# Performance work log

Measured on AMD Instinct MI355X. Metric: run time of the kernel, lower is better.

## Reference

```python
import jax, jax.numpy as jnp
import numpy as np

PATCH_SIZE = 3
CHANNELS = 1
SIGMA_RAW = 0.5
SIGMA_EFF = SIGMA_RAW * PATCH_SIZE ** 2  # sigma * patch_size**2 as in __init__


def setup_inputs() -> dict:
    key = jax.random.key(0)
    kx, ky = jax.random.split(key)
    N, C, H, W = 64, CHANNELS, 64, 64
    x = jax.random.normal(kx, (N, C, H, W), dtype=jnp.float32)
    y = jax.random.normal(ky, (N, C, H, W), dtype=jnp.float32)
    return {"x": x, "y": y}


def _pairwise_patch_distance(A, B):
    # A: (N_A, C, H, W), B: (N_B, C, H, W)
    N_A, C, H, W = A.shape
    N_B = B.shape[0]
    # broadcast pairwise squared pixel diffs: (N_A, N_B, C, H, W)
    pixel_diff = (A[:, None] - B[None]) ** 2
    kern = jnp.ones((1, C, PATCH_SIZE, PATCH_SIZE), dtype=A.dtype)  # OIHW
    d = jax.lax.conv_general_dilated(
        pixel_diff.reshape(N_A * N_B, C, H, W), kern,
        window_strides=(1, 1), padding='VALID',
        dimension_numbers=('NCHW', 'OIHW', 'NCHW'))
    H_new, W_new = d.shape[-2], d.shape[-1]
    return d.reshape(N_A, N_B, H_new, W_new)


def _gaussian_kernel(D):
    return jnp.exp(-D / (2.0 * SIGMA_EFF ** 2))


def _off_mean(K):
    # K: (N, N, h, w); mean over all off-diagonal (i != j) entries
    N, _, h, w = K.shape
    mask = ~jnp.eye(N, dtype=bool)
    total = jnp.sum(jnp.where(mask[:, :, None, None], K, jnp.zeros((), K.dtype)))
    count = (N * (N - 1)) * h * w
    return total / count


def reference(x, y):
    K_xx = _gaussian_kernel(_pairwise_patch_distance(x, x))
    K_xy = _gaussian_kernel(_pairwise_patch_distance(x, y))
    K_yy = _gaussian_kernel(_pairwise_patch_distance(y, y))
    return _off_mean(K_xx) - 2.0 * jnp.mean(K_xy) + _off_mean(K_yy)
```

## Files before the change

### kernel.cpp

```cpp
#include <hip/hip_runtime.h>
#include <hip/hip_fp16.h>


typedef __attribute__((ext_vector_type(4))) _Float16 half4v;
typedef __attribute__((ext_vector_type(4))) float f32x4;

#define NPOS 3844
#define WSTR 26
#define RSTR 20
#define NBLK 992

#define W_OFF (1.0 / (64.0 * 63.0 * 62.0 * 62.0))
#define W_ALL (1.0 / (64.0 * 64.0 * 62.0 * 62.0))

#if __has_builtin(__builtin_amdgcn_exp2f)
#define EXP2F(v) __builtin_amdgcn_exp2f(v)
#else
#define EXP2F(v) __expf((v) * 0.69314718055994530942f)
#endif

template<int CTRL>
__device__ __forceinline__ float dpp0_f(float v) {
    int r = __builtin_amdgcn_update_dpp(0, __float_as_int(v), CTRL, 0xf, 0xf, true);
    return __int_as_float(r);
}
template<int CTRL, int RM>
__device__ __forceinline__ float dppm_f(float v) {
    int r = __builtin_amdgcn_update_dpp(0, __float_as_int(v), CTRL, RM, 0xf, true);
    return __int_as_float(r);
}
__device__ __forceinline__ float wave_reduce_f(float v) {
    v += dpp0_f<0x111>(v);
    v += dpp0_f<0x112>(v);
    v += dpp0_f<0x114>(v);
    v += dpp0_f<0x118>(v);
    v += dppm_f<0x142, 0xa>(v);
    v += dppm_f<0x143, 0xc>(v);
    return v;
}
__device__ __forceinline__ unsigned short f16bits(float f) {
    __half h = __float2half(f);
    return *reinterpret_cast<unsigned short*>(&h);
}
__device__ __forceinline__ float f16tof(unsigned short u) {
    __half h = *reinterpret_cast<__half*>(&u);
    return __half2float(h);
}

__global__ __launch_bounds__(256, 4) void mmd_fused_kernel(
    const float* __restrict__ x, const float* __restrict__ y,
    float* __restrict__ part)
{
    const int t = threadIdx.x, wid = t >> 6, lane = t & 63;
    const int p  = blockIdx.x >> 4;
    const int qg = blockIdx.x & 15;
    const int q  = qg * 4 + wid;

    __shared__ unsigned short win[128 * WSTR];
    __shared__ unsigned short rec[4 * 128 * RSTR];
    __shared__ float pren[4 * 128];
    __shared__ float wred[3][4];

    const float NS   = -1.0f / (40.5f * 0.69314718055994530942f);
    const float M2NS = -2.0f * NS;

    {
        const int cg1 = (qg < 15) ? qg + 1 : 15;
        #pragma unroll
        for (int k = 0; k < 3; ++k) {
            int it = t + k * 256;
            int n = it / 6, rem = it % 6;
            int u = rem >> 1, cg = rem & 1;
            const float* img = (n < 64) ? (x + n * 4096) : (y + (n - 64) * 4096);
            float4 v = *reinterpret_cast<const float4*>(
                img + (p + u) * 64 + ((cg ? cg1 : qg) << 2));
            unsigned int d0 = f16bits(v.x) | ((unsigned)f16bits(v.y) << 16);
            unsigned int d1 = f16bits(v.z) | ((unsigned)f16bits(v.w) << 16);
            unsigned int* w32 = reinterpret_cast<unsigned int*>(
                &win[n * WSTR + u * 8 + cg * 4]);
            w32[0] = d0; w32[1] = d1;
        }
    }
    __syncthreads();

    #pragma unroll
    for (int k = 0; k < 2; ++k) {
        int rid = t + k * 256;
        int ql = rid >> 7, n = rid & 127;
        const unsigned short* wp = &win[n * WSTR + ql];
        unsigned short b[9];
        #pragma unroll
        for (int u = 0; u < 3; ++u) {
            b[u * 3 + 0] = wp[u * 8 + 0];
            b[u * 3 + 1] = wp[u * 8 + 1];
            b[u * 3 + 2] = wp[u * 8 + 2];
        }
        float pre = 0.f;
        #pragma unroll
        for (int e = 0; e < 9; ++e) {
            float fv = f16tof(b[e]);
            pre = fmaf(fv, fv, pre);
        }
        unsigned short* dp = &rec[(size_t)rid * RSTR];
        uint2 s0, s1, s2, s3;
        s0.x = b[0] | ((unsigned)b[1] << 16);
        s0.y = b[2] | ((unsigned)b[3] << 16);
        s1.x = b[4] | ((unsigned)b[5] << 16);
        s1.y = b[6] | ((unsigned)b[7] << 16);
        s2.x = (unsigned)b[8]; s2.y = 0u;
        s3.x = 0u;             s3.y = 0u;
        *reinterpret_cast<uint2*>(dp)      = s0;
        *reinterpret_cast<uint2*>(dp + 4)  = s1;
        *reinterpret_cast<uint2*>(dp + 8)  = s2;
        *reinterpret_cast<uint2*>(dp + 12) = s3;
        pren[rid] = pre * NS;
    }
    __syncthreads();

    const int r = lane & 15, kg = lane >> 4;
    half4v frag[8];
    #pragma unroll
    for (int g = 0; g < 8; ++g)
        frag[g] = *reinterpret_cast<const half4v*>(
            &rec[(size_t)(wid * 128 + g * 16 + r) * RSTR + kg * 4]);

    float pa[8][4], pb[8];
    #pragma unroll
    for (int g = 0; g < 8; ++g) {
        const float* pp = &pren[wid * 128 + g * 16 + kg * 4];
        pa[g][0] = pp[0]; pa[g][1] = pp[1]; pa[g][2] = pp[2]; pa[g][3] = pp[3];
        pb[g] = pren[wid * 128 + g * 16 + r];
    }

    const f32x4 zf = {0.f, 0.f, 0.f, 0.f};
    float ad0 = 0.f, ad1 = 0.f, as0 = 0.f, as1 = 0.f, ac0 = 0.f, ac1 = 0.f;

    #pragma unroll
    for (int g = 0; g < 8; ++g) {
        f32x4 c4 = __builtin_amdgcn_mfma_f32_16x16x16f16(frag[g], frag[g], zf, 0, 0, 0);
        float e = 0.f;
        #pragma unroll
        for (int m = 0; m < 4; ++m)
            e += EXP2F(fmaf(c4[m], M2NS, pa[g][m] + pb[g]));
        if (g & 1) ad1 += e; else ad0 += e;
    }

    #pragma unroll
    for (int ti = 1; ti < 8; ++ti)
        #pragma unroll
        for (int tj = 0; tj < ti; ++tj) {
            f32x4 c4 = __builtin_amdgcn_mfma_f32_16x16x16f16(frag[ti], frag[tj], zf, 0, 0, 0);
            float e = 0.f;
            #pragma unroll
            for (int m = 0; m < 4; ++m)
                e += EXP2F(fmaf(c4[m], M2NS, pa[ti][m] + pb[tj]));
            if (ti >= 4 && tj < 4) { if (tj & 1) ac1 += e; else ac0 += e; }
            else                   { if (tj & 1) as1 += e; else as0 += e; }
        }

    float acc_diag  = wave_reduce_f(ad0 + ad1);
    float acc_same  = wave_reduce_f(as0 + as1);
    float acc_cross = wave_reduce_f(ac0 + ac1);
    if (lane == 63) {
        const bool valid = (q < 62);
        wred[0][wid] = valid ? acc_diag  : 0.f;
        wred[1][wid] = valid ? acc_same  : 0.f;
        wred[2][wid] = valid ? acc_cross : 0.f;
    }
    __syncthreads();
    if (t == 0) {
        double sd = (double)((wred[0][0] + wred[0][1]) + (wred[0][2] + wred[0][3]));
        double ss = (double)((wred[1][0] + wred[1][1]) + (wred[1][2] + wred[1][3]));
        double sc = (double)((wred[2][0] + wred[2][1]) + (wred[2][2] + wred[2][3]));
        part[blockIdx.x] = (float)((sd + 2.0 * ss) * W_OFF - 2.0 * sc * W_ALL);
    }
}

__global__ __launch_bounds__(1024) void mmd_final_kernel(
    const float* __restrict__ part, float* __restrict__ out)
{
    const int t = threadIdx.x;
    double v = (t < NBLK) ? (double)part[t] : 0.0;
    #pragma unroll
    for (int off = 32; off > 0; off >>= 1)
        v += __shfl_xor(v, off);
    __shared__ double w[16];
    const int lane = t & 63, wd = t >> 6;
    if (lane == 0) w[wd] = v;
    __syncthreads();
    if (t == 0) {
        double S = 0.0;
        #pragma unroll
        for (int k = 0; k < 16; ++k) S += w[k];
        out[0] = (float)(S - 128.0 * (double)NPOS * W_OFF);
    }
}

extern "C" void kernel_launch(void* const* d_in, const int* in_sizes, int n_in,
                              void* d_out, int out_size, void* d_ws, size_t ws_size,
                              hipStream_t stream) {
    const float* x = (const float*)d_in[0];
    const float* y = (const float*)d_in[1];
    float* out  = (float*)d_out;
    float* part = (float*)d_ws;

    mmd_fused_kernel<<<NBLK, 256, 0, stream>>>(x, y, part);
    mmd_final_kernel<<<1, 1024, 0, stream>>>(part, out);
}
```

Measured before the change: 16.35 us.

## Split each column's triangular MFMA tile work across two waves per block

Doubles the block to 512 threads so two waves share each column position q. Each wave takes a balanced half of the lower-triangular 8x8 tile pairs (rows 0,1,6,7 vs 2,3,4,5, 18 tiles each). The load and record-build stages are redistributed over the larger block, and the final reduction sums eight wave partials instead of four. The aim is more parallel MFMA/exp work and shorter per-wave critical paths. The cost is more waves per block, duplicated fragment loads, and possible register and occupancy pressure at launch bounds (512,8).

```diff
diff --git a/kernel.cpp b/kernel.cpp
--- a/kernel.cpp
+++ b/kernel.cpp
@@ -47,19 +47,39 @@
     return __half2float(h);
 }
 
-__global__ __launch_bounds__(256, 4) void mmd_fused_kernel(
+template<int TI>
+__device__ __forceinline__ void do_ti(const half4v* frag, const float pa[8][4],
+                                      const float* pb, float M2NS,
+                                      float& ad, float& as, float& ac) {
+    const f32x4 zf = {0.f, 0.f, 0.f, 0.f};
+    #pragma unroll
+    for (int tj = 0; tj <= TI; ++tj) {
+        f32x4 c4 = __builtin_amdgcn_mfma_f32_16x16x16f16(frag[TI], frag[tj], zf, 0, 0, 0);
+        float e = 0.f;
+        #pragma unroll
+        for (int m = 0; m < 4; ++m)
+            e += EXP2F(fmaf(c4[m], M2NS, pa[TI][m] + pb[tj]));
+        if (tj == TI)                 ad += e;
+        else if (TI >= 4 && tj < 4)   ac += e;
+        else                          as += e;
+    }
+}
+
+__global__ __launch_bounds__(512, 8) void mmd_fused_kernel(
     const float* __restrict__ x, const float* __restrict__ y,
     float* __restrict__ part)
 {
     const int t = threadIdx.x, wid = t >> 6, lane = t & 63;
     const int p  = blockIdx.x >> 4;
     const int qg = blockIdx.x & 15;
-    const int q  = qg * 4 + wid;
+    const int pq = wid >> 1;
+    const int ws = wid & 1;
+    const int q  = qg * 4 + pq;
 
     __shared__ unsigned short win[128 * WSTR];
     __shared__ unsigned short rec[4 * 128 * RSTR];
     __shared__ float pren[4 * 128];
-    __shared__ float wred[3][4];
+    __shared__ float wred[3][8];
 
     const float NS   = -1.0f / (40.5f * 0.69314718055994530942f);
     const float M2NS = -2.0f * NS;
@@ -67,25 +87,26 @@
     {
         const int cg1 = (qg < 15) ? qg + 1 : 15;
         #pragma unroll
-        for (int k = 0; k < 3; ++k) {
-            int it = t + k * 256;
-            int n = it / 6, rem = it % 6;
-            int u = rem >> 1, cg = rem & 1;
-            const float* img = (n < 64) ? (x + n * 4096) : (y + (n - 64) * 4096);
-            float4 v = *reinterpret_cast<const float4*>(
-                img + (p + u) * 64 + ((cg ? cg1 : qg) << 2));
-            unsigned int d0 = f16bits(v.x) | ((unsigned)f16bits(v.y) << 16);
-            unsigned int d1 = f16bits(v.z) | ((unsigned)f16bits(v.w) << 16);
-            unsigned int* w32 = reinterpret_cast<unsigned int*>(
-                &win[n * WSTR + u * 8 + cg * 4]);
-            w32[0] = d0; w32[1] = d1;
-        }
-    }
-    __syncthreads();
-
-    #pragma unroll
-    for (int k = 0; k < 2; ++k) {
-        int rid = t + k * 256;
+        for (int k = 0; k < 2; ++k) {
+            int it = t + k * 512;
+            if (it < 768) {
+                int n = it / 6, rem = it % 6;
+                int u = rem >> 1, cg = rem & 1;
+                const float* img = (n < 64) ? (x + n * 4096) : (y + (n - 64) * 4096);
+                float4 v = *reinterpret_cast<const float4*>(
+                    img + (p + u) * 64 + ((cg ? cg1 : qg) << 2));
+                unsigned int d0 = f16bits(v.x) | ((unsigned)f16bits(v.y) << 16);
+                unsigned int d1 = f16bits(v.z) | ((unsigned)f16bits(v.w) << 16);
+                unsigned int* w32 = reinterpret_cast<unsigned int*>(
+                    &win[n * WSTR + u * 8 + cg * 4]);
+                w32[0] = d0; w32[1] = d1;
+            }
+        }
+    }
+    __syncthreads();
+
+    {
+        int rid = t;
         int ql = rid >> 7, n = rid & 127;
         const unsigned short* wp = &win[n * WSTR + ql];
         unsigned short b[9];
@@ -122,45 +143,32 @@
     #pragma unroll
     for (int g = 0; g < 8; ++g)
         frag[g] = *reinterpret_cast<const half4v*>(
-            &rec[(size_t)(wid * 128 + g * 16 + r) * RSTR + kg * 4]);
+            &rec[(size_t)(pq * 128 + g * 16 + r) * RSTR + kg * 4]);
 
     float pa[8][4], pb[8];
     #pragma unroll
     for (int g = 0; g < 8; ++g) {
-        const float* pp = &pren[wid * 128 + g * 16 + kg * 4];
+        const float* pp = &pren[pq * 128 + g * 16 + kg * 4];
         pa[g][0] = pp[0]; pa[g][1] = pp[1]; pa[g][2] = pp[2]; pa[g][3] = pp[3];
-        pb[g] = pren[wid * 128 + g * 16 + r];
-    }
-
-    const f32x4 zf = {0.f, 0.f, 0.f, 0.f};
-    float ad0 = 0.f, ad1 = 0.f, as0 = 0.f, as1 = 0.f, ac0 = 0.f, ac1 = 0.f;
-
-    #pragma unroll
-    for (int g = 0; g < 8; ++g) {
-        f32x4 c4 = __builtin_amdgcn_mfma_f32_16x16x16f16(frag[g], frag[g], zf, 0, 0, 0);
-        float e = 0.f;
-        #pragma unroll
-        for (int m = 0; m < 4; ++m)
-            e += EXP2F(fmaf(c4[m], M2NS, pa[g][m] + pb[g]));
-        if (g & 1) ad1 += e; else ad0 += e;
-    }
-
-    #pragma unroll
-    for (int ti = 1; ti < 8; ++ti)
-        #pragma unroll
-        for (int tj = 0; tj < ti; ++tj) {
-            f32x4 c4 = __builtin_amdgcn_mfma_f32_16x16x16f16(frag[ti], frag[tj], zf, 0, 0, 0);
-            float e = 0.f;
-            #pragma unroll
-            for (int m = 0; m < 4; ++m)
-                e += EXP2F(fmaf(c4[m], M2NS, pa[ti][m] + pb[tj]));
-            if (ti >= 4 && tj < 4) { if (tj & 1) ac1 += e; else ac0 += e; }
-            else                   { if (tj & 1) as1 += e; else as0 += e; }
-        }
-
-    float acc_diag  = wave_reduce_f(ad0 + ad1);
-    float acc_same  = wave_reduce_f(as0 + as1);
-    float acc_cross = wave_reduce_f(ac0 + ac1);
+        pb[g] = pren[pq * 128 + g * 16 + r];
+    }
+
+    float ad = 0.f, as = 0.f, ac = 0.f;
+    if (ws == 0) {
+        do_ti<0>(frag, pa, pb, M2NS, ad, as, ac);
+        do_ti<1>(frag, pa, pb, M2NS, ad, as, ac);
+        do_ti<6>(frag, pa, pb, M2NS, ad, as, ac);
+        do_ti<7>(frag, pa, pb, M2NS, ad, as, ac);
+    } else {
+        do_ti<2>(frag, pa, pb, M2NS, ad, as, ac);
+        do_ti<3>(frag, pa, pb, M2NS, ad, as, ac);
+        do_ti<4>(frag, pa, pb, M2NS, ad, as, ac);
+        do_ti<5>(frag, pa, pb, M2NS, ad, as, ac);
+    }
+
+    float acc_diag  = wave_reduce_f(ad);
+    float acc_same  = wave_reduce_f(as);
+    float acc_cross = wave_reduce_f(ac);
     if (lane == 63) {
         const bool valid = (q < 62);
         wred[0][wid] = valid ? acc_diag  : 0.f;
@@ -169,9 +177,12 @@
     }
     __syncthreads();
     if (t == 0) {
-        double sd = (double)((wred[0][0] + wred[0][1]) + (wred[0][2] + wred[0][3]));
-        double ss = (double)((wred[1][0] + wred[1][1]) + (wred[1][2] + wred[1][3]));
-        double sc = (double)((wred[2][0] + wred[2][1]) + (wred[2][2] + wred[2][3]));
+        float fd = 0.f, fs = 0.f, fc = 0.f;
+        #pragma unroll
+        for (int k = 0; k < 8; ++k) {
+            fd += wred[0][k]; fs += wred[1][k]; fc += wred[2][k];
+        }
+        double sd = (double)fd, ss = (double)fs, sc = (double)fc;
         part[blockIdx.x] = (float)((sd + 2.0 * ss) * W_OFF - 2.0 * sc * W_ALL);
     }
 }
@@ -204,6 +215,6 @@
     float* out  = (float*)d_out;
     float* part = (float*)d_ws;
 
-    mmd_fused_kernel<<<NBLK, 256, 0, stream>>>(x, y, part);
+    mmd_fused_kernel<<<NBLK, 512, 0, stream>>>(x, y, part);
     mmd_final_kernel<<<1, 1024, 0, stream>>>(part, out);
 }
```

New measurement: 19.01 us. 16.3% more time.

## Process two column groups per block with prefetched second window

Applied to the files above, without the earlier changes.

Each block now handles two adjacent column groups (qg pairs), halving the grid to 496 blocks. The global loads for the second window are issued before the first group's MFMA/exp work and written to a second LDS buffer afterward, overlapping load latency with compute. The change also amortizes per-block setup and partial-sum reduction, at the cost of less parallelism (about 2 blocks per CU) and more registers held across the loop.

```diff
diff --git a/kernel.cpp b/kernel.cpp
--- a/kernel.cpp
+++ b/kernel.cpp
@@ -8,7 +8,7 @@
 #define NPOS 3844
 #define WSTR 26
 #define RSTR 20
-#define NBLK 992
+#define NBLK 496
 
 #define W_OFF (1.0 / (64.0 * 63.0 * 62.0 * 62.0))
 #define W_ALL (1.0 / (64.0 * 64.0 * 62.0 * 62.0))
@@ -52,11 +52,11 @@
     float* __restrict__ part)
 {
     const int t = threadIdx.x, wid = t >> 6, lane = t & 63;
-    const int p  = blockIdx.x >> 4;
-    const int qg = blockIdx.x & 15;
-    const int q  = qg * 4 + wid;
-
-    __shared__ unsigned short win[128 * WSTR];
+    const int p    = blockIdx.x >> 3;
+    const int pair = blockIdx.x & 7;
+    const int qg0  = pair * 2;
+
+    __shared__ unsigned short win[2][128 * WSTR];
     __shared__ unsigned short rec[4 * 128 * RSTR];
     __shared__ float pren[4 * 128];
     __shared__ float wred[3][4];
@@ -64,108 +64,155 @@
     const float NS   = -1.0f / (40.5f * 0.69314718055994530942f);
     const float M2NS = -2.0f * NS;
 
+    const int sn  = t % 128;
+    (void)sn;
+
+    int s_n[3], s_u[3], s_cg[3];
+    #pragma unroll
+    for (int k = 0; k < 3; ++k) {
+        int it = t + k * 256;
+        s_n[k] = it / 6;
+        int rem = it % 6;
+        s_u[k]  = rem >> 1;
+        s_cg[k] = rem & 1;
+    }
+    const float* imgs[3];
+    #pragma unroll
+    for (int k = 0; k < 3; ++k)
+        imgs[k] = (s_n[k] < 64) ? (x + s_n[k] * 4096) : (y + (s_n[k] - 64) * 4096);
+
     {
-        const int cg1 = (qg < 15) ? qg + 1 : 15;
+        const int cg1 = qg0 + 1;
         #pragma unroll
         for (int k = 0; k < 3; ++k) {
-            int it = t + k * 256;
-            int n = it / 6, rem = it % 6;
-            int u = rem >> 1, cg = rem & 1;
-            const float* img = (n < 64) ? (x + n * 4096) : (y + (n - 64) * 4096);
             float4 v = *reinterpret_cast<const float4*>(
-                img + (p + u) * 64 + ((cg ? cg1 : qg) << 2));
+                imgs[k] + (p + s_u[k]) * 64 + ((s_cg[k] ? cg1 : qg0) << 2));
             unsigned int d0 = f16bits(v.x) | ((unsigned)f16bits(v.y) << 16);
             unsigned int d1 = f16bits(v.z) | ((unsigned)f16bits(v.w) << 16);
             unsigned int* w32 = reinterpret_cast<unsigned int*>(
-                &win[n * WSTR + u * 8 + cg * 4]);
+                &win[0][s_n[k] * WSTR + s_u[k] * 8 + s_cg[k] * 4]);
             w32[0] = d0; w32[1] = d1;
         }
     }
     __syncthreads();
 
-    #pragma unroll
-    for (int k = 0; k < 2; ++k) {
-        int rid = t + k * 256;
-        int ql = rid >> 7, n = rid & 127;
-        const unsigned short* wp = &win[n * WSTR + ql];
-        unsigned short b[9];
-        #pragma unroll
-        for (int u = 0; u < 3; ++u) {
-            b[u * 3 + 0] = wp[u * 8 + 0];
-            b[u * 3 + 1] = wp[u * 8 + 1];
-            b[u * 3 + 2] = wp[u * 8 + 2];
-        }
-        float pre = 0.f;
-        #pragma unroll
-        for (int e = 0; e < 9; ++e) {
-            float fv = f16tof(b[e]);
-            pre = fmaf(fv, fv, pre);
-        }
-        unsigned short* dp = &rec[(size_t)rid * RSTR];
-        uint2 s0, s1, s2, s3;
-        s0.x = b[0] | ((unsigned)b[1] << 16);
-        s0.y = b[2] | ((unsigned)b[3] << 16);
-        s1.x = b[4] | ((unsigned)b[5] << 16);
-        s1.y = b[6] | ((unsigned)b[7] << 16);
-        s2.x = (unsigned)b[8]; s2.y = 0u;
-        s3.x = 0u;             s3.y = 0u;
-        *reinterpret_cast<uint2*>(dp)      = s0;
-        *reinterpret_cast<uint2*>(dp + 4)  = s1;
-        *reinterpret_cast<uint2*>(dp + 8)  = s2;
-        *reinterpret_cast<uint2*>(dp + 12) = s3;
-        pren[rid] = pre * NS;
-    }
-    __syncthreads();
-
+    float ad_t = 0.f, as_t = 0.f, ac_t = 0.f;
     const int r = lane & 15, kg = lane >> 4;
-    half4v frag[8];
-    #pragma unroll
-    for (int g = 0; g < 8; ++g)
-        frag[g] = *reinterpret_cast<const half4v*>(
-            &rec[(size_t)(wid * 128 + g * 16 + r) * RSTR + kg * 4]);
-
-    float pa[8][4], pb[8];
-    #pragma unroll
-    for (int g = 0; g < 8; ++g) {
-        const float* pp = &pren[wid * 128 + g * 16 + kg * 4];
-        pa[g][0] = pp[0]; pa[g][1] = pp[1]; pa[g][2] = pp[2]; pa[g][3] = pp[3];
-        pb[g] = pren[wid * 128 + g * 16 + r];
-    }
-
-    const f32x4 zf = {0.f, 0.f, 0.f, 0.f};
-    float ad0 = 0.f, ad1 = 0.f, as0 = 0.f, as1 = 0.f, ac0 = 0.f, ac1 = 0.f;
-
-    #pragma unroll
-    for (int g = 0; g < 8; ++g) {
-        f32x4 c4 = __builtin_amdgcn_mfma_f32_16x16x16f16(frag[g], frag[g], zf, 0, 0, 0);
-        float e = 0.f;
-        #pragma unroll
-        for (int m = 0; m < 4; ++m)
-            e += EXP2F(fmaf(c4[m], M2NS, pa[g][m] + pb[g]));
-        if (g & 1) ad1 += e; else ad0 += e;
-    }
-
-    #pragma unroll
-    for (int ti = 1; ti < 8; ++ti)
-        #pragma unroll
-        for (int tj = 0; tj < ti; ++tj) {
-            f32x4 c4 = __builtin_amdgcn_mfma_f32_16x16x16f16(frag[ti], frag[tj], zf, 0, 0, 0);
+
+    #pragma unroll
+    for (int quad = 0; quad < 2; ++quad) {
+        const int qg = qg0 + quad;
+        const int q  = qg * 4 + wid;
+
+        #pragma unroll
+        for (int k = 0; k < 2; ++k) {
+            int rid = t + k * 256;
+            int ql = rid >> 7, n = rid & 127;
+            const unsigned short* wp = &win[quad][n * WSTR + ql];
+            unsigned short b[9];
+            #pragma unroll
+            for (int u = 0; u < 3; ++u) {
+                b[u * 3 + 0] = wp[u * 8 + 0];
+                b[u * 3 + 1] = wp[u * 8 + 1];
+                b[u * 3 + 2] = wp[u * 8 + 2];
+            }
+            float pre = 0.f;
+            #pragma unroll
+            for (int e = 0; e < 9; ++e) {
+                float fv = f16tof(b[e]);
+                pre = fmaf(fv, fv, pre);
+            }
+            unsigned short* dp = &rec[(size_t)rid * RSTR];
+            uint2 s0, s1, s2, s3;
+            s0.x = b[0] | ((unsigned)b[1] << 16);
+            s0.y = b[2] | ((unsigned)b[3] << 16);
+            s1.x = b[4] | ((unsigned)b[5] << 16);
+            s1.y = b[6] | ((unsigned)b[7] << 16);
+            s2.x = (unsigned)b[8]; s2.y = 0u;
+            s3.x = 0u;             s3.y = 0u;
+            *reinterpret_cast<uint2*>(dp)      = s0;
+            *reinterpret_cast<uint2*>(dp + 4)  = s1;
+            *reinterpret_cast<uint2*>(dp + 8)  = s2;
+            *reinterpret_cast<uint2*>(dp + 12) = s3;
+            pren[rid] = pre * NS;
+        }
+        __syncthreads();
+
+        half4v frag[8];
+        #pragma unroll
+        for (int g = 0; g < 8; ++g)
+            frag[g] = *reinterpret_cast<const half4v*>(
+                &rec[(size_t)(wid * 128 + g * 16 + r) * RSTR + kg * 4]);
+
+        float pa[8][4], pb[8];
+        #pragma unroll
+        for (int g = 0; g < 8; ++g) {
+            const float* pp = &pren[wid * 128 + g * 16 + kg * 4];
+            pa[g][0] = pp[0]; pa[g][1] = pp[1]; pa[g][2] = pp[2]; pa[g][3] = pp[3];
+            pb[g] = pren[wid * 128 + g * 16 + r];
+        }
+
+        float4 pf[3];
+        if (quad == 0) {
+            const int cg1 = qg0 + 2;
+            const int cg1c = (cg1 < 16) ? cg1 : 15;
+            #pragma unroll
+            for (int k = 0; k < 3; ++k)
+                pf[k] = *reinterpret_cast<const float4*>(
+                    imgs[k] + (p + s_u[k]) * 64 + ((s_cg[k] ? cg1c : (qg0 + 1)) << 2));
+        }
+
+        const f32x4 zf = {0.f, 0.f, 0.f, 0.f};
+        float ad0 = 0.f, ad1 = 0.f, as0 = 0.f, as1 = 0.f, ac0 = 0.f, ac1 = 0.f;
+
+        #pragma unroll
+        for (int g = 0; g < 8; ++g) {
+            f32x4 c4 = __builtin_amdgcn_mfma_f32_16x16x16f16(frag[g], frag[g], zf, 0, 0, 0);
             float e = 0.f;
             #pragma unroll
             for (int m = 0; m < 4; ++m)
-                e += EXP2F(fmaf(c4[m], M2NS, pa[ti][m] + pb[tj]));
-            if (ti >= 4 && tj < 4) { if (tj & 1) ac1 += e; else ac0 += e; }
-            else                   { if (tj & 1) as1 += e; else as0 += e; }
-        }
-
-    float acc_diag  = wave_reduce_f(ad0 + ad1);
-    float acc_same  = wave_reduce_f(as0 + as1);
-    float acc_cross = wave_reduce_f(ac0 + ac1);
+                e += EXP2F(fmaf(c4[m], M2NS, pa[g][m] + pb[g]));
+            if (g & 1) ad1 += e; else ad0 += e;
+        }
+        #pragma unroll
+        for (int ti = 1; ti < 8; ++ti)
+            #pragma unroll
+            for (int tj = 0; tj < ti; ++tj) {
+                f32x4 c4 = __builtin_amdgcn_mfma_f32_16x16x16f16(frag[ti], frag[tj], zf, 0, 0, 0);
+                float e = 0.f;
+                #pragma unroll
+                for (int m = 0; m < 4; ++m)
+                    e += EXP2F(fmaf(c4[m], M2NS, pa[ti][m] + pb[tj]));
+                if (ti >= 4 && tj < 4) { if (tj & 1) ac1 += e; else ac0 += e; }
+                else                   { if (tj & 1) as1 += e; else as0 += e; }
+            }
+
+        if (q < 62) {
+            ad_t += ad0 + ad1;
+            as_t += as0 + as1;
+            ac_t += ac0 + ac1;
+        }
+
+        if (quad == 0) {
+            #pragma unroll
+            for (int k = 0; k < 3; ++k) {
+                unsigned int d0 = f16bits(pf[k].x) | ((unsigned)f16bits(pf[k].y) << 16);
+                unsigned int d1 = f16bits(pf[k].z) | ((unsigned)f16bits(pf[k].w) << 16);
+                unsigned int* w32 = reinterpret_cast<unsigned int*>(
+                    &win[1][s_n[k] * WSTR + s_u[k] * 8 + s_cg[k] * 4]);
+                w32[0] = d0; w32[1] = d1;
+            }
+        }
+        __syncthreads();
+    }
+
+    float acc_diag  = wave_reduce_f(ad_t);
+    float acc_same  = wave_reduce_f(as_t);
+    float acc_cross = wave_reduce_f(ac_t);
     if (lane == 63) {
-        const bool valid = (q < 62);
-        wred[0][wid] = valid ? acc_diag  : 0.f;
-        wred[1][wid] = valid ? acc_same  : 0.f;
-        wred[2][wid] = valid ? acc_cross : 0.f;
+        wred[0][wid] = acc_diag;
+        wred[1][wid] = acc_same;
+        wred[2][wid] = acc_cross;
     }
     __syncthreads();
     if (t == 0) {
@@ -176,7 +223,7 @@
     }
 }
 
-__global__ __launch_bounds__(1024) void mmd_final_kernel(
+__global__ __launch_bounds__(512) void mmd_final_kernel(
     const float* __restrict__ part, float* __restrict__ out)
 {
     const int t = threadIdx.x;
@@ -184,14 +231,14 @@
     #pragma unroll
     for (int off = 32; off > 0; off >>= 1)
         v += __shfl_xor(v, off);
-    __shared__ double w[16];
+    __shared__ double w[8];
     const int lane = t & 63, wd = t >> 6;
     if (lane == 0) w[wd] = v;
     __syncthreads();
     if (t == 0) {
         double S = 0.0;
         #pragma unroll
-        for (int k = 0; k < 16; ++k) S += w[k];
+        for (int k = 0; k < 8; ++k) S += w[k];
         out[0] = (float)(S - 128.0 * (double)NPOS * W_OFF);
     }
 }
@@ -205,5 +252,5 @@
     float* part = (float*)d_ws;
 
     mmd_fused_kernel<<<NBLK, 256, 0, stream>>>(x, y, part);
-    mmd_final_kernel<<<1, 1024, 0, stream>>>(part, out);
-}
+    mmd_final_kernel<<<1, 512, 0, stream>>>(part, out);
+}
```

Result: no change. 16.28 us (-0.4%).
